# Performance work log

Hardware: AMD Instinct MI355X
Metric: run time of the kernel (lower is better)

Reference implementation:

```python
import jax, jax.numpy as jnp
import numpy as np

N, E, F_NODE, F_EDGE, H = 50000, 800000, 64, 32, 64
NT, ET, ETE = 3, 4, 4  # num node types, num edge types, edge-type embedding dim
NEG = 0.2              # leaky_relu negative slope (PyG HEATConv default)


def hetero_lin(x, t, W, b):
    # per-type linear: x [N,in], t [N] int, W [T,in,out], b [T,out]
    outs = jnp.einsum('ni,tio->tno', x, W) + b[:, None, :]   # [T,N,out]
    return outs[t, jnp.arange(x.shape[0])]                   # [N,out]


def segment_softmax(logits, seg, num_segments):
    m = jax.ops.segment_max(logits, seg, num_segments=num_segments)
    ex = jnp.exp(logits - m[seg])
    s = jax.ops.segment_sum(ex, seg, num_segments=num_segments)
    return ex / (s[seg] + 1e-16)


def eheat_conv(x, src, dst, node_type, edge_type, edge_attr, Whl, bhl, Ete, Wea, Watt, Wlin):
    n = x.shape[0]
    h = hetero_lin(x, node_type, Whl, bhl)            # [N,H]
    ete = jax.nn.leaky_relu(Ete[edge_type], NEG)      # [E,ETE]
    ea = jax.nn.leaky_relu(edge_attr @ Wea, NEG)      # [E,H] edge embedding (returned)
    xi, xj = h[dst], h[src]                           # gather target/source node feats
    # attention logits = leaky_relu(att(cat([x_i, x_j, ete, ea]))); Watt split to avoid big concat
    Wi, Wj, Wt, We = Watt[:H], Watt[H:2 * H], Watt[2 * H:2 * H + ETE], Watt[2 * H + ETE:]
    logits = jax.nn.leaky_relu(xi @ Wi + xj @ Wj + ete @ Wt + ea @ We, NEG)[:, 0]  # [E]
    alpha = segment_softmax(logits, dst, n)           # softmax over incoming edges of dst
    # message = lin(cat([x_j, ea])) * alpha ; scatter-add at dst (heads=1, dropout eval=identity)
    msg = (xj @ Wlin[:H] + ea @ Wlin[H:]) * alpha[:, None]   # [E,H]
    out = jax.ops.segment_sum(msg, dst, num_segments=n)     # [N,H]
    return out, ea


def setup_inputs():
    key = jax.random.key(0)
    ks = jax.random.split(key, 40)
    def rnd(i, shape):
        return jax.random.normal(ks[i], shape, dtype=jnp.float32) * 0.1
    inp = {
        'x': jax.random.normal(ks[0], (N, F_NODE), dtype=jnp.float32),
        'edge_index': jax.random.randint(ks[1], (2, E), 0, N),
        'node_type': jax.random.randint(ks[2], (N,), 0, NT),
        'edge_type': jax.random.randint(ks[3], (E,), 0, ET),
        'edge_attr': jax.random.normal(ks[4], (E, F_EDGE), dtype=jnp.float32),
    }
    node_ins = [F_NODE, H, H]
    edge_ins = [F_EDGE, H, H]
    i = 5
    for l in range(3):
        inp[f'Whl{l+1}'] = rnd(i, (NT, node_ins[l], H)); i += 1
        inp[f'bhl{l+1}'] = jnp.zeros((NT, H), jnp.float32)
        inp[f'Ete{l+1}'] = rnd(i, (ET, ETE)); i += 1
        inp[f'Wea{l+1}'] = rnd(i, (edge_ins[l], H)); i += 1
        inp[f'Watt{l+1}'] = rnd(i, (2 * H + ETE + H, 1)); i += 1
        inp[f'Wlin{l+1}'] = rnd(i, (2 * H, H)); i += 1
    inp['Wnc'] = rnd(i, (NT, H, 1)); i += 1
    inp['bnc'] = jnp.zeros((NT, 1), jnp.float32)
    inp['Wec'] = rnd(i, (ET, H, 1)); i += 1
    inp['bec'] = jnp.zeros((ET, 1), jnp.float32)
    return inp


def reference(x, edge_index, node_type, edge_type, edge_attr,
              Whl1, bhl1, Ete1, Wea1, Watt1, Wlin1,
              Whl2, bhl2, Ete2, Wea2, Watt2, Wlin2,
              Whl3, bhl3, Ete3, Wea3, Watt3, Wlin3,
              Wnc, bnc, Wec, bec):
    src, dst = edge_index[0], edge_index[1]
    h, e = eheat_conv(x, src, dst, node_type, edge_type, edge_attr,
                      Whl1, bhl1, Ete1, Wea1, Watt1, Wlin1)
    h, e = jax.nn.relu(h), jax.nn.relu(e)   # dropout is identity in eval mode
    h, e = eheat_conv(h, src, dst, node_type, edge_type, e,
                      Whl2, bhl2, Ete2, Wea2, Watt2, Wlin2)
    h, e = jax.nn.relu(h), jax.nn.relu(e)
    h, e = eheat_conv(h, src, dst, node_type, edge_type, e,
                      Whl3, bhl3, Ete3, Wea3, Watt3, Wlin3)
    h, e = jax.nn.relu(h), jax.nn.relu(e)
    x_out = hetero_lin(h, node_type, Wnc, bnc)   # [N,1]
    e_out = hetero_lin(e, edge_type, Wec, bec)   # [E,1]
    return (x_out, e_out)
```

## Files before the change

kernel.cpp:

```cpp
#include <hip/hip_runtime.h>
#include <hip/hip_bf16.h>

#define NEG 0.2f
#define LRELU(x) ((x) > 0.f ? (x) : NEG*(x))

typedef __hip_bfloat16 bf16;
typedef __attribute__((ext_vector_type(8))) short short8v;
typedef __attribute__((ext_vector_type(4))) float f32x4;

__device__ __forceinline__ float b2f(bf16 v){ return __bfloat162float(v); }
__device__ __forceinline__ float ldf(const float* p, size_t i){ return p[i]; }
__device__ __forceinline__ float ldf(const bf16* p, size_t i){ return __bfloat162float(p[i]); }

__device__ __forceinline__ float wred(float v){
#pragma unroll
  for(int o=32;o>0;o>>=1) v += __shfl_down(v,o);
  return v;
}

__device__ __forceinline__ int atomAddI(int* p, int v){
  return __hip_atomic_fetch_add(p, v, __ATOMIC_RELAXED, __HIP_MEMORY_SCOPE_AGENT);
}


__global__ __launch_bounds__(256) void k_hist(
    const int* __restrict__ dst, int* __restrict__ deg, int nE)
{
  int e = blockIdx.x*blockDim.x + threadIdx.x;
  if (e >= nE) return;
  atomAddI(&deg[dst[e]], 1);
}

__global__ __launch_bounds__(1024) void k_scan(
    const int* __restrict__ deg, int* __restrict__ off, int nN)
{
  __shared__ int part[1024];
  int tid = threadIdx.x;
  int chunk = (nN + 1023) / 1024;
  int lo = tid*chunk, hi = min((tid+1)*chunk, nN);
  int s = 0;
  for (int i=lo;i<hi;i++) s += deg[i];
  part[tid] = s;
  __syncthreads();
  for (int d=1; d<1024; d<<=1){
    int v = (tid>=d) ? part[tid-d] : 0;
    __syncthreads();
    part[tid] += v;
    __syncthreads();
  }
  int run = (tid==0) ? 0 : part[tid-1];
  for (int i=lo;i<hi;i++){ off[i] = run; run += deg[i]; }
  if (tid==1023) off[nN] = part[1023];
}

__global__ __launch_bounds__(256) void k_scatter(
    const int* __restrict__ dst, const int* __restrict__ off,
    int* __restrict__ cnt, int* __restrict__ eid, int nE)
{
  int e = blockIdx.x*blockDim.x + threadIdx.x;
  if (e >= nE) return;
  int d = dst[e];
  int p = atomAddI(&cnt[d], 1);
  eid[off[d] + p] = e;
}

__global__ __launch_bounds__(256) void k_perm(
    const int* __restrict__ eid, const int* __restrict__ src,
    const int* __restrict__ dst, const int* __restrict__ ety,
    int* __restrict__ srcP, int* __restrict__ dstP, int* __restrict__ etyP, int nE)
{
  int i = blockIdx.x*blockDim.x + threadIdx.x;
  if (i >= nE) return;
  int e = eid[i];
  srcP[i] = src[e];
  dstP[i] = dst[e];
  etyP[i] = ety[e];
}


template<typename TIN, bool RELU_IN>
__global__ __launch_bounds__(256) void k_hlin(
    const TIN* __restrict__ xin, const int* __restrict__ ntype,
    const float* __restrict__ Whl, const float* __restrict__ bhl,
    const float* __restrict__ Watt,
    bf16* __restrict__ h, float* __restrict__ hi_s, float* __restrict__ hj_s,
    int nN)
{
  int wid  = (blockIdx.x*blockDim.x + threadIdx.x) >> 6;
  int lane = threadIdx.x & 63;
  if (wid >= nN) return;
  int t = ntype[wid];
  float xv = ldf(xin, (size_t)wid*64 + lane);
  if (RELU_IN) xv = fmaxf(xv, 0.f);
  const float* W = Whl + (size_t)t*4096;
  float acc = bhl[t*64 + lane];
#pragma unroll
  for (int i=0;i<64;i++) acc = fmaf(__shfl(xv, i), W[i*64 + lane], acc);
  h[(size_t)wid*64 + lane] = __float2bfloat16(acc);
  float pi = wred(acc * Watt[lane]);
  float pj = wred(acc * Watt[64 + lane]);
  if (lane==0){ hi_s[wid]=pi; hj_s[wid]=pj; }
}

__global__ __launch_bounds__(256) void k_bfrag(
    const float* __restrict__ W, bf16* __restrict__ frag, int KS)
{
  int t = blockIdx.x*blockDim.x + threadIdx.x;
  int total = 4*KS*64;
  if (t >= total) return;
  int lane = t & 63;
  int ks = (t>>6) % KS;
  int nt = (t>>6) / KS;
  int kb = lane>>4, col = lane&15;
#pragma unroll
  for (int j=0;j<8;j++){
    frag[((size_t)(nt*KS+ks)*64 + lane)*8 + j] =
      __float2bfloat16(W[(ks*32 + kb*8 + j)*64 + nt*16 + col]);
  }
}

template<int LAYER>
__global__ __launch_bounds__(256) void k_ea_mfma(
    const void* __restrict__ ain_, const int* __restrict__ eid,
    const bf16* __restrict__ bfrag, const float* __restrict__ Watt,
    const int* __restrict__ srcP, const int* __restrict__ dstP,
    const int* __restrict__ etyP, const float* __restrict__ Ete,
    const float* __restrict__ hi_s, const float* __restrict__ hj_s,
    bf16* __restrict__ eaS, float* __restrict__ exS,
    const float* __restrict__ Wec, const float* __restrict__ bec,
    float* __restrict__ e_out, int nE)
{
  constexpr int KS = (LAYER==0) ? 1 : 2;
  int wid  = (blockIdx.x*blockDim.x + threadIdx.x) >> 6;
  int lane = threadIdx.x & 63;
  int e0 = wid * 16;
  if (e0 >= nE) return;
  int row = lane & 15;
  int kb  = lane >> 4;
  int er  = min(e0 + row, nE-1);

  short8v a[KS];
  if (LAYER==0) {
    const float* A = (const float*)ain_;
    const float* p = A + (size_t)eid[er]*32 + kb*8;
#pragma unroll
    for (int j=0;j<8;j++){
      bf16 b = __float2bfloat16(p[j]);
      a[0][j] = *reinterpret_cast<short*>(&b);
    }
  } else {
    const bf16* A = (const bf16*)ain_;
#pragma unroll
    for (int ks=0; ks<KS; ks++){
      short8v v = *reinterpret_cast<const short8v*>(
          reinterpret_cast<const short*>(A + (size_t)er*64 + ks*32 + kb*8));
#pragma unroll
      for (int j=0;j<8;j++) v[j] = (v[j] & (short)0x8000) ? (short)0 : v[j];
      a[ks] = v;
    }
  }

  f32x4 acc[4];
#pragma unroll
  for (int nt=0; nt<4; nt++){
    f32x4 c = {0.f,0.f,0.f,0.f};
#pragma unroll
    for (int ks=0; ks<KS; ks++){
      short8v b = *reinterpret_cast<const short8v*>(
          reinterpret_cast<const short*>(bfrag) + (((size_t)nt*KS + ks)*64 + lane)*8);
      c = __builtin_amdgcn_mfma_f32_16x16x32_bf16(a[ks], b, c, 0, 0, 0);
    }
#pragma unroll
    for (int r=0;r<4;r++) c[r] = LRELU(c[r]);
    acc[nt] = c;
  }

#pragma unroll
  for (int r=0;r<4;r++){
    int e = e0 + kb*4 + r;
    if (e < nE){
#pragma unroll
      for (int nt=0;nt<4;nt++)
        eaS[(size_t)e*64 + nt*16 + row] = __float2bfloat16(acc[nt][r]);
    }
  }

#pragma unroll
  for (int r=0;r<4;r++){
    int e = e0 + kb*4 + r;
    bool valid = (e < nE);
    int t = valid ? etyP[e] : 0;
    float lp = 0.f, pe = 0.f;
#pragma unroll
    for (int nt=0;nt<4;nt++) lp = fmaf(acc[nt][r], Watt[132 + nt*16 + row], lp);
    if (LAYER==2){
#pragma unroll
      for (int nt=0;nt<4;nt++) pe = fmaf(fmaxf(acc[nt][r],0.f), Wec[t*64 + nt*16 + row], pe);
    }
#pragma unroll
    for (int m=1;m<16;m<<=1){
      lp += __shfl_xor(lp, m);
      if (LAYER==2) pe += __shfl_xor(pe, m);
    }
    if (row == 0 && valid){
      int d = dstP[e], s = srcP[e];
      float wt = 0.f;
#pragma unroll
      for (int k=0;k<4;k++){ float v = Ete[t*4+k]; v = LRELU(v); wt = fmaf(v, Watt[128+k], wt); }
      float l = lp + hi_s[d] + hj_s[s] + wt;
      l = LRELU(l);
      exS[e] = __expf(fminf(l, 60.f));
      if (LAYER==2) e_out[eid[e]] = pe + bec[t];
    }
  }
}

__global__ __launch_bounds__(256) void k_agg(
    const int* __restrict__ off, const int* __restrict__ srcP,
    const bf16* __restrict__ h, const bf16* __restrict__ eaS,
    const float* __restrict__ exS,
    bf16* __restrict__ uv, int nN)
{
  int wid  = (blockIdx.x*blockDim.x + threadIdx.x) >> 6;
  int lane = threadIdx.x & 63;
  if (wid >= nN) return;
  int beg = off[wid], end = off[wid+1];
  float au = 0.f, av = 0.f, ss = 0.f;
  int i = beg;
  int sC = 0; float aC = 0.f;
  if (i < end){ sC = srcP[i]; aC = exS[i]; }
  while (i < end){
    int s = sC; float a = aC;
    int j = i + 1;
    if (j < end){ sC = srcP[j]; aC = exS[j]; }
    float hv = b2f(h[(size_t)s*64 + lane]);
    float ev = b2f(eaS[(size_t)i*64 + lane]);
    au = fmaf(a, hv, au);
    av = fmaf(a, ev, av);
    ss += a;
    i = j;
  }
  float inv = 1.f / (ss + 1e-16f);
  uv[(size_t)wid*128 + lane]      = __float2bfloat16(au * inv);
  uv[(size_t)wid*128 + 64 + lane] = __float2bfloat16(av * inv);
}

__global__ __launch_bounds__(256) void k_mm_mfma(
    const bf16* __restrict__ uv, const bf16* __restrict__ bfrag,
    float* __restrict__ out, int nN)
{
  int wid  = (blockIdx.x*blockDim.x + threadIdx.x) >> 6;
  int lane = threadIdx.x & 63;
  int n0 = wid * 16;
  if (n0 >= nN) return;
  int row = lane & 15;
  int kb  = lane >> 4;
  int nr  = min(n0 + row, nN-1);

  short8v a[4];
#pragma unroll
  for (int ks=0; ks<4; ks++)
    a[ks] = *reinterpret_cast<const short8v*>(
        reinterpret_cast<const short*>(uv + (size_t)nr*128 + ks*32 + kb*8));

  f32x4 acc[4];
#pragma unroll
  for (int nt=0; nt<4; nt++){
    f32x4 c = {0.f,0.f,0.f,0.f};
#pragma unroll
    for (int ks=0; ks<4; ks++){
      short8v b = *reinterpret_cast<const short8v*>(
          reinterpret_cast<const short*>(bfrag) + (((size_t)nt*4 + ks)*64 + lane)*8);
      c = __builtin_amdgcn_mfma_f32_16x16x32_bf16(a[ks], b, c, 0, 0, 0);
    }
    acc[nt] = c;
  }

#pragma unroll
  for (int r=0;r<4;r++){
    int n = n0 + kb*4 + r;
    if (n < nN){
#pragma unroll
      for (int nt=0;nt<4;nt++)
        out[(size_t)n*64 + nt*16 + row] = acc[nt][r];
    }
  }
}

__global__ __launch_bounds__(256) void k_xout(
    const float* __restrict__ hin, const int* __restrict__ ntype,
    const float* __restrict__ Wnc, const float* __restrict__ bnc,
    float* __restrict__ xout, int nN)
{
  int wid  = (blockIdx.x*blockDim.x + threadIdx.x) >> 6;
  int lane = threadIdx.x & 63;
  if (wid >= nN) return;
  int t = ntype[wid];
  float v = fmaxf(hin[(size_t)wid*64 + lane], 0.f);
  float p = wred(v * Wnc[t*64 + lane]);
  if (lane==0) xout[wid] = p + bnc[t];
}

extern "C" void kernel_launch(void* const* d_in, const int* in_sizes, int n_in,
                              void* d_out, int out_size, void* d_ws, size_t ws_size,
                              hipStream_t stream) {
  const float* x      = (const float*)d_in[0];
  const int*   eidx   = (const int*) d_in[1];
  const int*   ntype  = (const int*) d_in[2];
  const int*   etype  = (const int*) d_in[3];
  const float* eattr  = (const float*)d_in[4];
  const float* Whl[3]  = {(const float*)d_in[5],  (const float*)d_in[11], (const float*)d_in[17]};
  const float* bhl[3]  = {(const float*)d_in[6],  (const float*)d_in[12], (const float*)d_in[18]};
  const float* Ete[3]  = {(const float*)d_in[7],  (const float*)d_in[13], (const float*)d_in[19]};
  const float* Wea[3]  = {(const float*)d_in[8],  (const float*)d_in[14], (const float*)d_in[20]};
  const float* Watt[3] = {(const float*)d_in[9],  (const float*)d_in[15], (const float*)d_in[21]};
  const float* Wlin[3] = {(const float*)d_in[10], (const float*)d_in[16], (const float*)d_in[22]};
  const float* Wnc = (const float*)d_in[23];
  const float* bnc = (const float*)d_in[24];
  const float* Wec = (const float*)d_in[25];
  const float* bec = (const float*)d_in[26];

  const int nN = in_sizes[2];
  const int nE = in_sizes[3];
  const int* srcI = eidx;
  const int* dstI = eidx + nE;

  float* ws = (float*)d_ws;
  size_t o = 0;
  bf16*  h      = (bf16*)(ws + o); o += (size_t)nN*32;
  float* outA   = ws + o;
  bf16*  uv     = (bf16*)(ws + o); o += (size_t)nN*64;
  float* hi_s   = ws + o;          o += (size_t)nN;
  float* hj_s   = ws + o;          o += (size_t)nN;
  float* exS    = ws + o;          o += (size_t)nE;
  bf16*  eaS    = (bf16*)(ws + o); o += (size_t)nE*32;
  int*   deg    = (int*)(ws + o);  o += (size_t)nN;
  int*   off    = (int*)(ws + o);  o += (size_t)nN + 1;
  int*   eid    = (int*)(ws + o);  o += (size_t)nE;
  int*   srcP   = (int*)(ws + o);  o += (size_t)nE;
  int*   dstP   = (int*)(ws + o);  o += (size_t)nE;
  int*   etyP   = (int*)(ws + o);  o += (size_t)nE;
  o = (o + 3) & ~(size_t)3;
  bf16*  bfrag  = (bf16*)(ws + o); o += (size_t)4096;

  dim3 blk(256);
  int nodeWB = (int)(((size_t)nN*64 + 255)/256);
  int edgeTB = (nE + 255)/256;
  int eaMB   = (int)(((size_t)((nE+15)/16)*64 + 255)/256);
  int mmMB   = (int)(((size_t)((nN+15)/16)*64 + 255)/256);

  hipMemsetAsync(deg, 0, (size_t)nN*4, stream);
  k_hist<<<edgeTB, blk, 0, stream>>>(dstI, deg, nE);
  k_scan<<<1, 1024, 0, stream>>>(deg, off, nN);
  hipMemsetAsync(deg, 0, (size_t)nN*4, stream);
  k_scatter<<<edgeTB, blk, 0, stream>>>(dstI, off, deg, eid, nE);
  k_perm<<<edgeTB, blk, 0, stream>>>(eid, srcI, dstI, etype, srcP, dstP, etyP, nE);

  float* xout = (float*)d_out;

  for (int L = 0; L < 3; ++L) {
    if (L == 0)
      k_hlin<float,false><<<nodeWB, blk, 0, stream>>>(x,    ntype, Whl[L], bhl[L], Watt[L], h, hi_s, hj_s, nN);
    else
      k_hlin<float,true ><<<nodeWB, blk, 0, stream>>>(outA, ntype, Whl[L], bhl[L], Watt[L], h, hi_s, hj_s, nN);

    int KS = (L==0) ? 1 : 2;
    k_bfrag<<<(4*KS*64 + 255)/256, blk, 0, stream>>>(Wea[L], bfrag, KS);
    if (L == 0)
      k_ea_mfma<0><<<eaMB, blk, 0, stream>>>(eattr, eid, bfrag, Watt[L], srcP, dstP, etyP, Ete[L],
                                             hi_s, hj_s, eaS, exS, nullptr, nullptr, nullptr, nE);
    else if (L == 1)
      k_ea_mfma<1><<<eaMB, blk, 0, stream>>>(eaS, eid, bfrag, Watt[L], srcP, dstP, etyP, Ete[L],
                                             hi_s, hj_s, eaS, exS, nullptr, nullptr, nullptr, nE);
    else
      k_ea_mfma<2><<<eaMB, blk, 0, stream>>>(eaS, eid, bfrag, Watt[L], srcP, dstP, etyP, Ete[L],
                                             hi_s, hj_s, eaS, exS, Wec, bec, xout + nN, nE);

    k_agg<<<nodeWB, blk, 0, stream>>>(off, srcP, h, eaS, exS, uv, nN);

    k_bfrag<<<(4*4*64 + 255)/256, blk, 0, stream>>>(Wlin[L], bfrag, 4);
    k_mm_mfma<<<mmMB, blk, 0, stream>>>(uv, bfrag, outA, nN);
  }

  k_xout<<<nodeWB, blk, 0, stream>>>(outA, ntype, Wnc, bnc, xout, nN);
}
```

Baseline: 928.6 us.

## Process two edge tiles per wave, unroll aggregation, fuse final classifier

The edge-embedding MFMA kernel now handles 32 edges per wave, two 16-row tiles, and reuses each B fragment load across both tiles. The aggregation loop is unrolled by two with independent loads in place of the software-prefetch loop, which exposes more memory-level parallelism. The final node classifier is fused into the last matmul kernel, so the separate k_xout launch and the write and read of outA are removed. In exchange, register pressure rises in the edge kernel and fewer waves are launched for it.

Result: no change. 913.1 us (-1.7%).

```diff
diff --git a/kernel.cpp b/kernel.cpp
--- a/kernel.cpp
+++ b/kernel.cpp
@@ -133,84 +133,94 @@
   constexpr int KS = (LAYER==0) ? 1 : 2;
   int wid  = (blockIdx.x*blockDim.x + threadIdx.x) >> 6;
   int lane = threadIdx.x & 63;
-  int e0 = wid * 16;
+  int e0 = wid * 32;
   if (e0 >= nE) return;
   int row = lane & 15;
   int kb  = lane >> 4;
-  int er  = min(e0 + row, nE-1);
-
-  short8v a[KS];
-  if (LAYER==0) {
-    const float* A = (const float*)ain_;
-    const float* p = A + (size_t)eid[er]*32 + kb*8;
-#pragma unroll
-    for (int j=0;j<8;j++){
-      bf16 b = __float2bfloat16(p[j]);
-      a[0][j] = *reinterpret_cast<short*>(&b);
-    }
-  } else {
-    const bf16* A = (const bf16*)ain_;
-#pragma unroll
-    for (int ks=0; ks<KS; ks++){
-      short8v v = *reinterpret_cast<const short8v*>(
-          reinterpret_cast<const short*>(A + (size_t)er*64 + ks*32 + kb*8));
-#pragma unroll
-      for (int j=0;j<8;j++) v[j] = (v[j] & (short)0x8000) ? (short)0 : v[j];
-      a[ks] = v;
-    }
-  }
-
-  f32x4 acc[4];
+
+  short8v a[2][KS];
+#pragma unroll
+  for (int tl=0; tl<2; tl++){
+    int er = min(e0 + tl*16 + row, nE-1);
+    if (LAYER==0) {
+      const float* A = (const float*)ain_;
+      const float* p = A + (size_t)eid[er]*32 + kb*8;
+#pragma unroll
+      for (int j=0;j<8;j++){
+        bf16 b = __float2bfloat16(p[j]);
+        a[tl][0][j] = *reinterpret_cast<short*>(&b);
+      }
+    } else {
+      const bf16* A = (const bf16*)ain_;
+#pragma unroll
+      for (int ks=0; ks<KS; ks++){
+        short8v v = *reinterpret_cast<const short8v*>(
+            reinterpret_cast<const short*>(A + (size_t)er*64 + ks*32 + kb*8));
+#pragma unroll
+        for (int j=0;j<8;j++) v[j] = (v[j] & (short)0x8000) ? (short)0 : v[j];
+        a[tl][ks] = v;
+      }
+    }
+  }
+
+  f32x4 acc[2][4];
 #pragma unroll
   for (int nt=0; nt<4; nt++){
-    f32x4 c = {0.f,0.f,0.f,0.f};
+    f32x4 c0 = {0.f,0.f,0.f,0.f}, c1 = {0.f,0.f,0.f,0.f};
 #pragma unroll
     for (int ks=0; ks<KS; ks++){
       short8v b = *reinterpret_cast<const short8v*>(
           reinterpret_cast<const short*>(bfrag) + (((size_t)nt*KS + ks)*64 + lane)*8);
-      c = __builtin_amdgcn_mfma_f32_16x16x32_bf16(a[ks], b, c, 0, 0, 0);
-    }
-#pragma unroll
-    for (int r=0;r<4;r++) c[r] = LRELU(c[r]);
-    acc[nt] = c;
-  }
-
-#pragma unroll
-  for (int r=0;r<4;r++){
-    int e = e0 + kb*4 + r;
-    if (e < nE){
-#pragma unroll
-      for (int nt=0;nt<4;nt++)
-        eaS[(size_t)e*64 + nt*16 + row] = __float2bfloat16(acc[nt][r]);
-    }
-  }
-
-#pragma unroll
-  for (int r=0;r<4;r++){
-    int e = e0 + kb*4 + r;
-    bool valid = (e < nE);
-    int t = valid ? etyP[e] : 0;
-    float lp = 0.f, pe = 0.f;
-#pragma unroll
-    for (int nt=0;nt<4;nt++) lp = fmaf(acc[nt][r], Watt[132 + nt*16 + row], lp);
-    if (LAYER==2){
-#pragma unroll
-      for (int nt=0;nt<4;nt++) pe = fmaf(fmaxf(acc[nt][r],0.f), Wec[t*64 + nt*16 + row], pe);
-    }
-#pragma unroll
-    for (int m=1;m<16;m<<=1){
-      lp += __shfl_xor(lp, m);
-      if (LAYER==2) pe += __shfl_xor(pe, m);
-    }
-    if (row == 0 && valid){
-      int d = dstP[e], s = srcP[e];
-      float wt = 0.f;
-#pragma unroll
-      for (int k=0;k<4;k++){ float v = Ete[t*4+k]; v = LRELU(v); wt = fmaf(v, Watt[128+k], wt); }
-      float l = lp + hi_s[d] + hj_s[s] + wt;
-      l = LRELU(l);
-      exS[e] = __expf(fminf(l, 60.f));
-      if (LAYER==2) e_out[eid[e]] = pe + bec[t];
+      c0 = __builtin_amdgcn_mfma_f32_16x16x32_bf16(a[0][ks], b, c0, 0, 0, 0);
+      c1 = __builtin_amdgcn_mfma_f32_16x16x32_bf16(a[1][ks], b, c1, 0, 0, 0);
+    }
+#pragma unroll
+    for (int r=0;r<4;r++){ c0[r] = LRELU(c0[r]); c1[r] = LRELU(c1[r]); }
+    acc[0][nt] = c0; acc[1][nt] = c1;
+  }
+
+#pragma unroll
+  for (int tl=0; tl<2; tl++){
+#pragma unroll
+    for (int r=0;r<4;r++){
+      int e = e0 + tl*16 + kb*4 + r;
+      if (e < nE){
+#pragma unroll
+        for (int nt=0;nt<4;nt++)
+          eaS[(size_t)e*64 + nt*16 + row] = __float2bfloat16(acc[tl][nt][r]);
+      }
+    }
+  }
+
+#pragma unroll
+  for (int tl=0; tl<2; tl++){
+#pragma unroll
+    for (int r=0;r<4;r++){
+      int e = e0 + tl*16 + kb*4 + r;
+      bool valid = (e < nE);
+      int t = valid ? etyP[e] : 0;
+      float lp = 0.f, pe = 0.f;
+#pragma unroll
+      for (int nt=0;nt<4;nt++) lp = fmaf(acc[tl][nt][r], Watt[132 + nt*16 + row], lp);
+      if (LAYER==2){
+#pragma unroll
+        for (int nt=0;nt<4;nt++) pe = fmaf(fmaxf(acc[tl][nt][r],0.f), Wec[t*64 + nt*16 + row], pe);
+      }
+#pragma unroll
+      for (int m=1;m<16;m<<=1){
+        lp += __shfl_xor(lp, m);
+        if (LAYER==2) pe += __shfl_xor(pe, m);
+      }
+      if (row == 0 && valid){
+        int d = dstP[e], s = srcP[e];
+        float wt = 0.f;
+#pragma unroll
+        for (int k=0;k<4;k++){ float v = Ete[t*4+k]; v = LRELU(v); wt = fmaf(v, Watt[128+k], wt); }
+        float l = lp + hi_s[d] + hj_s[s] + wt;
+        l = LRELU(l);
+        exS[e] = __expf(fminf(l, 60.f));
+        if (LAYER==2) e_out[eid[e]] = pe + bec[t];
+      }
     }
   }
 }
@@ -227,27 +237,33 @@
   int beg = off[wid], end = off[wid+1];
   float au = 0.f, av = 0.f, ss = 0.f;
   int i = beg;
-  int sC = 0; float aC = 0.f;
-  if (i < end){ sC = srcP[i]; aC = exS[i]; }
-  while (i < end){
-    int s = sC; float a = aC;
-    int j = i + 1;
-    if (j < end){ sC = srcP[j]; aC = exS[j]; }
-    float hv = b2f(h[(size_t)s*64 + lane]);
-    float ev = b2f(eaS[(size_t)i*64 + lane]);
-    au = fmaf(a, hv, au);
-    av = fmaf(a, ev, av);
+  for (; i+1 < end; i += 2){
+    int   s0 = srcP[i],   s1 = srcP[i+1];
+    float a0 = exS[i],    a1 = exS[i+1];
+    float h0 = b2f(h[(size_t)s0*64 + lane]);
+    float h1 = b2f(h[(size_t)s1*64 + lane]);
+    float v0 = b2f(eaS[(size_t)i*64 + lane]);
+    float v1 = b2f(eaS[(size_t)(i+1)*64 + lane]);
+    au = fmaf(a0, h0, au); av = fmaf(a0, v0, av); ss += a0;
+    au = fmaf(a1, h1, au); av = fmaf(a1, v1, av); ss += a1;
+  }
+  if (i < end){
+    int s = srcP[i]; float a = exS[i];
+    au = fmaf(a, b2f(h[(size_t)s*64 + lane]), au);
+    av = fmaf(a, b2f(eaS[(size_t)i*64 + lane]), av);
     ss += a;
-    i = j;
   }
   float inv = 1.f / (ss + 1e-16f);
   uv[(size_t)wid*128 + lane]      = __float2bfloat16(au * inv);
   uv[(size_t)wid*128 + 64 + lane] = __float2bfloat16(av * inv);
 }
 
+template<bool FINAL>
 __global__ __launch_bounds__(256) void k_mm_mfma(
     const bf16* __restrict__ uv, const bf16* __restrict__ bfrag,
-    float* __restrict__ out, int nN)
+    float* __restrict__ out,
+    const int* __restrict__ ntype, const float* __restrict__ Wnc,
+    const float* __restrict__ bnc, float* __restrict__ xout, int nN)
 {
   int wid  = (blockIdx.x*blockDim.x + threadIdx.x) >> 6;
   int lane = threadIdx.x & 63;
@@ -276,29 +292,31 @@
     acc[nt] = c;
   }
 
-#pragma unroll
-  for (int r=0;r<4;r++){
-    int n = n0 + kb*4 + r;
-    if (n < nN){
+  if (!FINAL){
+#pragma unroll
+    for (int r=0;r<4;r++){
+      int n = n0 + kb*4 + r;
+      if (n < nN){
+#pragma unroll
+        for (int nt=0;nt<4;nt++)
+          out[(size_t)n*64 + nt*16 + row] = acc[nt][r];
+      }
+    }
+  } else {
+#pragma unroll
+    for (int r=0;r<4;r++){
+      int n = n0 + kb*4 + r;
+      bool valid = (n < nN);
+      int t = valid ? ntype[n] : 0;
+      float pe = 0.f;
 #pragma unroll
       for (int nt=0;nt<4;nt++)
-        out[(size_t)n*64 + nt*16 + row] = acc[nt][r];
-    }
-  }
-}
-
-__global__ __launch_bounds__(256) void k_xout(
-    const float* __restrict__ hin, const int* __restrict__ ntype,
-    const float* __restrict__ Wnc, const float* __restrict__ bnc,
-    float* __restrict__ xout, int nN)
-{
-  int wid  = (blockIdx.x*blockDim.x + threadIdx.x) >> 6;
-  int lane = threadIdx.x & 63;
-  if (wid >= nN) return;
-  int t = ntype[wid];
-  float v = fmaxf(hin[(size_t)wid*64 + lane], 0.f);
-  float p = wred(v * Wnc[t*64 + lane]);
-  if (lane==0) xout[wid] = p + bnc[t];
+        pe = fmaf(fmaxf(acc[nt][r],0.f), Wnc[t*64 + nt*16 + row], pe);
+#pragma unroll
+      for (int m=1;m<16;m<<=1) pe += __shfl_xor(pe, m);
+      if (row == 0 && valid) xout[n] = pe + bnc[t];
+    }
+  }
 }
 
 extern "C" void kernel_launch(void* const* d_in, const int* in_sizes, int n_in,
@@ -346,7 +364,7 @@
   dim3 blk(256);
   int nodeWB = (int)(((size_t)nN*64 + 255)/256);
   int edgeTB = (nE + 255)/256;
-  int eaMB   = (int)(((size_t)((nE+15)/16)*64 + 255)/256);
+  int eaMB   = (int)(((size_t)((nE+31)/32)*64 + 255)/256);
   int mmMB   = (int)(((size_t)((nN+15)/16)*64 + 255)/256);
 
   hipMemsetAsync(deg, 0, (size_t)nN*4, stream);
@@ -379,8 +397,9 @@
     k_agg<<<nodeWB, blk, 0, stream>>>(off, srcP, h, eaS, exS, uv, nN);
 
     k_bfrag<<<(4*4*64 + 255)/256, blk, 0, stream>>>(Wlin[L], bfrag, 4);
-    k_mm_mfma<<<mmMB, blk, 0, stream>>>(uv, bfrag, outA, nN);
-  }
-
-  k_xout<<<nodeWB, blk, 0, stream>>>(outA, ntype, Wnc, bnc, xout, nN);
-}
+    if (L < 2)
+      k_mm_mfma<false><<<mmMB, blk, 0, stream>>>(uv, bfrag, outA, nullptr, nullptr, nullptr, nullptr, nN);
+    else
+      k_mm_mfma<true ><<<mmMB, blk, 0, stream>>>(uv, bfrag, nullptr, ntype, Wnc, bnc, xout, nN);
+  }
+}
```
